# Kernel tuning notes

Measured on AMD Instinct MI355X. Metric: run time of the kernel, lower is better.

Reference implementation:

```python
import jax, jax.numpy as jnp
import numpy as np
from jax import lax

T, S = 2000, 100          # trees, nodes per tree
N = T * S                 # total nodes
F = 256                   # in_feats (sent_hidden_size)
H = 256                   # h_feats (prop_hidden_size)


def _build_forest():
    # Random recursive forest: node j in each tree attaches to a uniform earlier node.
    rng = np.random.default_rng(0)
    pl = np.zeros((T, S), np.int64)    # local parent index
    dep = np.zeros((T, S), np.int64)
    rows = np.arange(T)
    for j in range(1, S):
        p = rng.integers(0, j, size=T)
        pl[:, j] = p
        dep[:, j] = dep[rows, p] + 1
    depth = dep.ravel()
    parent = (np.arange(T)[:, None] * S + pl).ravel()
    is_root = (np.arange(N) % S) == 0
    kids = np.arange(N)[~is_root]
    par = parent[~is_root]
    order = np.argsort(par, kind='stable')
    kids_s, par_s = kids[order], par[order]
    counts = np.bincount(par_s, minlength=N)
    C = int(counts.max())
    offsets = np.concatenate([[0], np.cumsum(counts)])
    pos = np.arange(len(kids_s)) - offsets[par_s]
    ch_all = np.full((N, C), N + 1, np.int32)   # pad with dummy zero-hidden row N+1
    ch_all[par_s, pos] = kids_s
    maxd = int(depth.max())
    L = maxd  # processed layers: depths 0..maxd-1 (deepest leaves stay zero, as in torch)
    layer_lists = [np.where(depth == d)[0] for d in range(L)]
    M = max(len(l) for l in layer_lists)
    layer_nodes = np.full((L, M), N, np.int32)  # pad writes to scratch row N
    child_idx = np.full((L, M, C), N + 1, np.int32)
    child_cnt = np.zeros((L, M), np.int32)
    for d, nd in enumerate(layer_lists):
        m = len(nd)
        layer_nodes[d, :m] = nd
        child_idx[d, :m] = ch_all[nd]
        child_cnt[d, :m] = counts[nd]
    root_idx = (np.arange(T) * S).astype(np.int32)
    return layer_nodes, child_idx, child_cnt, root_idx


def setup_inputs() -> dict:
    layer_nodes, child_idx, child_cnt, root_idx = _build_forest()
    key = jax.random.key(0)
    k1, k2, k3, k4, k5 = jax.random.split(key, 5)
    bound = 1.0 / np.sqrt(H)  # torch GRUCell default init
    u = lambda kk, sh: jax.random.uniform(kk, sh, jnp.float32, -bound, bound)
    return {
        'inputs': jax.random.normal(k1, (N, F), jnp.float32),
        'w_ih': u(k2, (3 * H, F)),
        'w_hh': u(k3, (3 * H, H)),
        'b_ih': u(k4, (3 * H,)),
        'b_hh': u(k5, (3 * H,)),
        'layer_nodes': jnp.asarray(layer_nodes),
        'child_idx': jnp.asarray(child_idx),
        'child_cnt': jnp.asarray(child_cnt),
        'root_idx': jnp.asarray(root_idx),
    }


def _gru(x, h, w_ih, w_hh, b_ih, b_hh):
    gi = x @ w_ih.T + b_ih
    gh = h @ w_hh.T + b_hh
    ir, iz, ig = jnp.split(gi, 3, axis=-1)
    hr, hz, hg = jnp.split(gh, 3, axis=-1)
    r = jax.nn.sigmoid(ir + hr)
    z = jax.nn.sigmoid(iz + hz)
    n = jnp.tanh(ig + r * hg)
    return (1.0 - z) * n + z * h


def _forward(inputs, w_ih, w_hh, b_ih, b_hh, layer_nodes, child_idx, child_cnt, root_idx):
    # rows N (scatter scratch for padded slots) and N+1 (always-zero child pad) appended
    x_all = jnp.concatenate([inputs, jnp.zeros((2, F), inputs.dtype)], axis=0)
    h0 = jnp.zeros((N + 2, H), inputs.dtype)

    def step(all_h, layer):
        nodes, cidx, ccnt = layer
        ch = all_h[cidx]                                        # [M, C, H]
        denom = jnp.maximum(ccnt, 1).astype(all_h.dtype)[:, None]
        h_prev = ch.sum(axis=1) / denom                         # mean over children; 0 for leaves
        new_h = _gru(x_all[nodes], h_prev, w_ih, w_hh, b_ih, b_hh)
        return all_h.at[nodes].set(new_h), None

    # process deepest layer first (reversed(range(max_depth)) in the original)
    xs = (layer_nodes[::-1], child_idx[::-1], child_cnt[::-1])
    all_h, _ = lax.scan(step, h0, xs)
    return all_h[root_idx]                                      # [T, H]


def reference(inputs, w_ih, w_hh, b_ih, b_hh, layer_nodes, child_idx, child_cnt, root_idx):
    return _forward(inputs, w_ih, w_hh, b_ih, b_hh, layer_nodes, child_idx, child_cnt, root_idx)
```

## Files before the change

kernel.cpp:

```cpp
#include <hip/hip_runtime.h>
#include <hip/hip_bf16.h>
#include <math.h>

#define N_NODES 200000
#define T_TREES 2000
#define S_NODES 100
#define F_DIM 256
#define H_DIM 256
#define G_DIM 768
#define D_MAX 24

typedef __attribute__((ext_vector_type(8))) short short8b;
typedef __attribute__((ext_vector_type(4))) float f32x4;

static __device__ __forceinline__ unsigned short f2bf(float x) {
    union { __hip_bfloat16 h; unsigned short u; } cv;
    cv.h = __float2bfloat16(x);
    return cv.u;
}
static __device__ __forceinline__ float bf2f(unsigned short u) {
    return __uint_as_float(((unsigned)u) << 16);
}
static __device__ __forceinline__ float fsig(float x) {
    return __builtin_amdgcn_rcpf(1.0f + __expf(-x));
}
static __device__ __forceinline__ float ftanh(float x) {
    return 1.0f - 2.0f * __builtin_amdgcn_rcpf(__expf(2.0f * x) + 1.0f);
}

__global__ void k_zero(float4* __restrict__ p, int n4) {
    float4 z = make_float4(0.f, 0.f, 0.f, 0.f);
    for (int i = blockIdx.x * blockDim.x + threadIdx.x; i < n4;
         i += gridDim.x * blockDim.x)
        p[i] = z;
}

__global__ void k_convx(const float* __restrict__ x, unsigned short* __restrict__ xb,
                        int n8) {
    for (int i = blockIdx.x * blockDim.x + threadIdx.x; i < n8;
         i += gridDim.x * blockDim.x) {
        const float4* px = (const float4*)(x + (size_t)i * 8);
        float4 u = px[0], v = px[1];
        short8b t;
        t[0] = f2bf(u.x); t[1] = f2bf(u.y); t[2] = f2bf(u.z); t[3] = f2bf(u.w);
        t[4] = f2bf(v.x); t[5] = f2bf(v.y); t[6] = f2bf(v.z); t[7] = f2bf(v.w);
        *(short8b*)(xb + (size_t)i * 8) = t;
    }
}

__global__ void k_findM(const int* __restrict__ ln, int LM, int* __restrict__ Mdev) {
    int local = 0x7F7F7F7F;
    for (int p = T_TREES + blockIdx.x * blockDim.x + threadIdx.x; p < LM;
         p += gridDim.x * blockDim.x)
        if (ln[p] < N_NODES && p < local) local = p;
#pragma unroll
    for (int off = 32; off; off >>= 1) {
        int o = __shfl_down(local, off);
        if (o < local) local = o;
    }
    __shared__ int wmin[4];
    if ((threadIdx.x & 63) == 0) wmin[threadIdx.x >> 6] = local;
    __syncthreads();
    if (threadIdx.x == 0) {
        int m = wmin[0];
        for (int i = 1; i < 4; ++i) if (wmin[i] < m) m = wmin[i];
        if (m < 0x7F7F7F7F) atomicMin(Mdev, m);
    }
}

__global__ void k_compact(const int* __restrict__ ln,
                          const int* __restrict__ child_cnt,
                          const int* __restrict__ Mdev,
                          int* __restrict__ int_cnt,
                          int* __restrict__ int_pos,
                          int LM) {
    const int M = Mdev[0];
    const int lane = threadIdx.x & 63;
    for (int p = blockIdx.x * blockDim.x + threadIdx.x;
         p < ((LM + 63) & ~63);
         p += gridDim.x * blockDim.x) {
        const bool inb = (p < LM);
        const int d = inb ? (p / M) : 0;
        const bool pred = inb && (ln[p] < N_NODES) &&
                          (child_cnt[p] > 0 || p < M) && d < D_MAX;
        unsigned long long remaining = __ballot(pred);
        while (remaining) {
            const int leader = (int)__ffsll((long long)remaining) - 1;
            const int dd = __shfl(d, leader);
            const unsigned long long grp = __ballot(pred && d == dd);
            int base = 0;
            if (lane == leader)
                base = atomicAdd(&int_cnt[dd], (int)__popcll(grp));
            base = __shfl(base, leader);
            if (pred && d == dd) {
                int rank = (int)__popcll(grp & ((1ULL << lane) - 1ULL));
                int_pos[(size_t)dd * M + base + rank] = p;
            }
            remaining &= ~grp;
        }
    }
}

__global__ void k_convw(const float* __restrict__ wi, const float* __restrict__ wh,
                        unsigned short* __restrict__ wib, unsigned short* __restrict__ whb) {
    int i = blockIdx.x * blockDim.x + threadIdx.x;
    if (i < G_DIM * F_DIM) {
        wib[i] = f2bf(wi[i]);
        whb[i] = f2bf(wh[i]);
    }
}

__global__ __launch_bounds__(256) void k_gemm_x(
    const unsigned short* __restrict__ xb,
    const unsigned short* __restrict__ wib,
    const float* __restrict__ b_ih,
    unsigned short* __restrict__ gi_all) {
    __shared__ unsigned short Bs[2][64][256];

    const int tid = threadIdx.x;
    const int wv = tid >> 6, lane = tid & 63;
    const int lr = lane & 15, kg = lane >> 4;
    const long m0 = (long)blockIdx.x * 128 + wv * 32;

    short8b A[2][8];
#pragma unroll
    for (int ms = 0; ms < 2; ++ms) {
        long r = m0 + ms * 16 + lr;
        if (r > N_NODES - 1) r = N_NODES - 1;
        const unsigned short* xp = xb + r * F_DIM + kg * 8;
#pragma unroll
        for (int ks = 0; ks < 8; ++ks)
            A[ms][ks] = *(const short8b*)(xp + ks * 32);
    }

    const int sr = tid >> 2, sp = tid & 3;
    const int hs = (sr & 3) | (((sr >> 3) & 1) << 2);
    const int gp_off = (lr >> 2) * 8 + (lr & 3);
    const int hq = (lr & 3) | (((lr >> 2) & 1) << 2);

    short8b st[8];
    {
        const unsigned short* src = wib + (size_t)sr * F_DIM;
#pragma unroll
        for (int q = 0; q < 4; ++q) {
            int c = sp * 16 + q * 64;
            st[2 * q]     = *(const short8b*)(src + c);
            st[2 * q + 1] = *(const short8b*)(src + c + 8);
        }
#pragma unroll
        for (int q = 0; q < 4; ++q) {
            int c0 = sp * 2 + q * 8, c1 = c0 + 1;
            *(short8b*)&Bs[0][sr][((c0 & 24) | ((c0 ^ hs) & 7)) << 3] = st[2 * q];
            *(short8b*)&Bs[0][sr][((c1 & 24) | ((c1 ^ hs) & 7)) << 3] = st[2 * q + 1];
        }
    }
    __syncthreads();

    const f32x4 zf = {0.f, 0.f, 0.f, 0.f};

    for (int nt = 0; nt < 12; ++nt) {
        const int cur = nt & 1;
        if (nt < 11) {
            const unsigned short* src = wib + (size_t)((nt + 1) * 64 + sr) * F_DIM;
#pragma unroll
            for (int q = 0; q < 4; ++q) {
                int c = sp * 16 + q * 64;
                st[2 * q]     = *(const short8b*)(src + c);
                st[2 * q + 1] = *(const short8b*)(src + c + 8);
            }
        }
#pragma unroll
        for (int nsp = 0; nsp < 2; ++nsp) {
            f32x4 aP0 = zf, aQ0 = zf, aP1 = zf, aQ1 = zf;
            const int rP = nsp * 32 + gp_off;
#pragma unroll
            for (int ks = 0; ks < 8; ++ks) {
                const int c = ks * 4 + kg;
                const int pc = ((c & 24) | ((c ^ hq) & 7)) << 3;
                short8b BP = *(const short8b*)&Bs[cur][rP][pc];
                short8b BQ = *(const short8b*)&Bs[cur][rP + 4][pc];
                aP0 = __builtin_amdgcn_mfma_f32_16x16x32_bf16(BP, A[0][ks], aP0, 0, 0, 0);
                aQ0 = __builtin_amdgcn_mfma_f32_16x16x32_bf16(BQ, A[0][ks], aQ0, 0, 0, 0);
                aP1 = __builtin_amdgcn_mfma_f32_16x16x32_bf16(BP, A[1][ks], aP1, 0, 0, 0);
                aQ1 = __builtin_amdgcn_mfma_f32_16x16x32_bf16(BQ, A[1][ks], aQ1, 0, 0, 0);
            }
            const int g0 = nt * 64 + nsp * 32 + kg * 8;
            f32x4 b0 = *(const f32x4*)(b_ih + g0);
            f32x4 b1 = *(const f32x4*)(b_ih + g0 + 4);
            long m = m0 + lr;
            if (m < N_NODES) {
                short8b pk;
#pragma unroll
                for (int i = 0; i < 4; ++i) {
                    pk[i]     = f2bf(aP0[i] + b0[i]);
                    pk[4 + i] = f2bf(aQ0[i] + b1[i]);
                }
                *(short8b*)(gi_all + m * G_DIM + g0) = pk;
            }
            m = m0 + 16 + lr;
            if (m < N_NODES) {
                short8b pk;
#pragma unroll
                for (int i = 0; i < 4; ++i) {
                    pk[i]     = f2bf(aP1[i] + b0[i]);
                    pk[4 + i] = f2bf(aQ1[i] + b1[i]);
                }
                *(short8b*)(gi_all + m * G_DIM + g0) = pk;
            }
        }
        if (nt < 11) {
            __syncthreads();
#pragma unroll
            for (int q = 0; q < 4; ++q) {
                int c0 = sp * 2 + q * 8, c1 = c0 + 1;
                *(short8b*)&Bs[cur ^ 1][sr][((c0 & 24) | ((c0 ^ hs) & 7)) << 3] = st[2 * q];
                *(short8b*)&Bs[cur ^ 1][sr][((c1 & 24) | ((c1 ^ hs) & 7)) << 3] = st[2 * q + 1];
            }
            __syncthreads();
        }
    }
}

__global__ void k_leaf(const int* __restrict__ ln,
                       const int* __restrict__ child_cnt,
                       const int* __restrict__ Mdev,
                       const unsigned short* __restrict__ gi_all,
                       const float* __restrict__ b_hh,
                       unsigned short* __restrict__ h_all,
                       int LM) {
    const int M = Mdev[0];
    const int total = LM * 8;
    for (int t = blockIdx.x * blockDim.x + threadIdx.x; t < total;
         t += gridDim.x * blockDim.x) {
        const int p = t >> 3;
        if (p < M) continue;
        const int node = ln[p];
        if (node >= N_NODES || child_cnt[p] != 0) continue;
        const int cb = (t & 7) * 32;
        const unsigned short* gp = gi_all + (size_t)node * G_DIM;
        unsigned short* hw = h_all + (size_t)node * H_DIM;
#pragma unroll
        for (int q = 0; q < 4; ++q) {
            const int k = cb + q * 8;
            short8b gr = *(const short8b*)(gp + k);
            short8b gz = *(const short8b*)(gp + 256 + k);
            short8b gn = *(const short8b*)(gp + 512 + k);
            f32x4 br0 = *(const f32x4*)(b_hh + k);
            f32x4 br1 = *(const f32x4*)(b_hh + k + 4);
            f32x4 bz0 = *(const f32x4*)(b_hh + 256 + k);
            f32x4 bz1 = *(const f32x4*)(b_hh + 256 + k + 4);
            f32x4 bn0 = *(const f32x4*)(b_hh + 512 + k);
            f32x4 bn1 = *(const f32x4*)(b_hh + 512 + k + 4);
            short8b ph;
#pragma unroll
            for (int j = 0; j < 8; ++j) {
                float bhr = (j < 4) ? br0[j] : br1[j - 4];
                float bhz = (j < 4) ? bz0[j] : bz1[j - 4];
                float bhn = (j < 4) ? bn0[j] : bn1[j - 4];
                float r = fsig(bf2f((unsigned short)gr[j]) + bhr);
                float z = fsig(bf2f((unsigned short)gz[j]) + bhz);
                float n = ftanh(bf2f((unsigned short)gn[j]) + r * bhn);
                ph[j] = f2bf((1.0f - z) * n);
            }
            *(short8b*)(hw + k) = ph;
        }
    }
}

#define LOADC2(buf, ns_, kh_)                                                  \
  _Pragma("unroll")                                                            \
  for (int kk = 0; kk < 4; ++kk)                                               \
    buf[kk] = *(const short8b*)(whb +                                          \
        (size_t)(512 + cb + (ns_) * 16 + lr) * H_DIM + ((kh_) * 4 + kk) * 32 + kg * 8);

#define MMACP(c_)                                                              \
  _Pragma("unroll")                                                            \
  for (int ks = 0; ks < 8; ++ks) {                                             \
    const int cch = ks * 4 + kg;                                               \
    const int pc = ((cch & 24) | ((cch ^ lr) & 7)) << 3;                       \
    short8b A0 = *(const short8b*)&Ab[lr][pc];                                 \
    short8b A1 = *(const short8b*)&Ab[16 + lr][pc];                            \
    _Pragma("unroll")                                                          \
    for (int ns = 0; ns < 2; ++ns) {                                           \
      acc[c_][0][ns] = __builtin_amdgcn_mfma_f32_16x16x32_bf16(                \
          A0, Bp[c_][ns][ks], acc[c_][0][ns], 0, 0, 0);                        \
      acc[c_][1][ns] = __builtin_amdgcn_mfma_f32_16x16x32_bf16(                \
          A1, Bp[c_][ns][ks], acc[c_][1][ns], 0, 0, 0);                        \
    }                                                                          \
  }

#define MMAC2(buf, ns_, kh_)                                                   \
  _Pragma("unroll")                                                            \
  for (int kk = 0; kk < 4; ++kk) {                                             \
    const int ks = (kh_) * 4 + kk;                                             \
    const int cch = ks * 4 + kg;                                               \
    const int pc = ((cch & 24) | ((cch ^ lr) & 7)) << 3;                       \
    short8b A0 = *(const short8b*)&Ab[lr][pc];                                 \
    short8b A1 = *(const short8b*)&Ab[16 + lr][pc];                            \
    acc[2][0][ns_] = __builtin_amdgcn_mfma_f32_16x16x32_bf16(                  \
        A0, buf[kk], acc[2][0][ns_], 0, 0, 0);                                 \
    acc[2][1][ns_] = __builtin_amdgcn_mfma_f32_16x16x32_bf16(                  \
        A1, buf[kk], acc[2][1][ns_], 0, 0, 0);                                 \
  }

__global__ __launch_bounds__(512, 2) void k_layer(
    const int* __restrict__ layer_nodes,
    const int* __restrict__ child_idx,
    const int* __restrict__ child_cnt,
    const int* __restrict__ Mdev,
    const int* __restrict__ int_cnt,
    const int* __restrict__ int_pos,
    const unsigned short* __restrict__ whb,
    const unsigned short* __restrict__ gi_all,
    const float* __restrict__ b_hh,
    unsigned short* __restrict__ h_all,
    float* __restrict__ out,
    int d, int C) {
    __shared__ unsigned short Ab[32][256];
    __shared__ unsigned short Ag[32][776];
    __shared__ int Nd[32];

    const int icnt = int_cnt[d];
    if (icnt == 0) return;
    const int M = Mdev[0];
    const int ntiles = (icnt + 31) >> 5;
    if (blockIdx.x >= ntiles) return;
    const long pbase = (long)d * M;

    const int tid = threadIdx.x;
    const int wv = tid >> 6, lane = tid & 63;
    const int lr = lane & 15, kg = lane >> 4;
    const int cb = wv * 32;

    short8b Bp[2][2][8];
#pragma unroll
    for (int c = 0; c < 2; ++c)
#pragma unroll
        for (int ns = 0; ns < 2; ++ns) {
            const unsigned short* bp =
                whb + (size_t)(c * 256 + cb + ns * 16 + lr) * H_DIM + kg * 8;
#pragma unroll
            for (int ks = 0; ks < 8; ++ks)
                Bp[c][ns][ks] = *(const short8b*)(bp + ks * 32);
        }

    float bh[3][2];
#pragma unroll
    for (int c = 0; c < 3; ++c)
#pragma unroll
        for (int ns = 0; ns < 2; ++ns)
            bh[c][ns] = b_hh[c * 256 + cb + ns * 16 + lr];

    const int srow = tid >> 4;
    const int sc = tid & 15;

    for (int tile = blockIdx.x; tile < ntiles; tile += gridDim.x) {
        __syncthreads();
        {
            int slot = tile * 32 + srow;
            int p = (slot < icnt) ? int_pos[pbase + slot] : -1;
            int node = (p >= 0) ? layer_nodes[p] : -1;
            if (sc == 0) Nd[srow] = node;
            {
                const unsigned short* gp =
                    gi_all + (size_t)(node >= 0 ? node : 0) * G_DIM;
#pragma unroll
                for (int pass = 0; pass < 6; ++pass) {
                    int col = sc * 8 + pass * 128;
                    *(short8b*)&Ag[srow][col] = *(const short8b*)(gp + col);
                }
            }
            int cc = 0;
            const int* ch = nullptr;
            if (p >= 0) {
                cc = child_cnt[p];
                ch = child_idx + (size_t)p * C;
            }
            float inv = 1.0f / (float)(cc > 0 ? cc : 1);
            float sum[16];
#pragma unroll
            for (int i = 0; i < 16; ++i) sum[i] = 0.f;
#pragma unroll 2
            for (int c = 0; c < cc; ++c) {
                int kid = ch[c];
                const unsigned short* hr = h_all + (size_t)kid * H_DIM + sc * 16;
                short8b v0 = *(const short8b*)hr;
                short8b v1 = *(const short8b*)(hr + 8);
#pragma unroll
                for (int i = 0; i < 8; ++i) {
                    sum[i]     += bf2f((unsigned short)v0[i]);
                    sum[8 + i] += bf2f((unsigned short)v1[i]);
                }
            }
            short8b q0, q1;
#pragma unroll
            for (int i = 0; i < 8; ++i) {
                q0[i] = f2bf(sum[i] * inv);
                q1[i] = f2bf(sum[8 + i] * inv);
            }
            const int g = srow & 7;
            const int c0 = 2 * sc, c1 = 2 * sc + 1;
            *(short8b*)&Ab[srow][((c0 & 24) | ((c0 ^ g) & 7)) << 3] = q0;
            *(short8b*)&Ab[srow][((c1 & 24) | ((c1 ^ g) & 7)) << 3] = q1;
        }
        __syncthreads();

        const f32x4 zf = {0.f, 0.f, 0.f, 0.f};
        f32x4 acc[3][2][2];
#pragma unroll
        for (int c = 0; c < 3; ++c)
#pragma unroll
            for (int ms = 0; ms < 2; ++ms)
#pragma unroll
                for (int ns = 0; ns < 2; ++ns) acc[c][ms][ns] = zf;

        short8b C2a[4], C2b[4];
        LOADC2(C2a, 0, 0);
        MMACP(0);
        LOADC2(C2b, 0, 1);
        MMAC2(C2a, 0, 0);
        LOADC2(C2a, 1, 0);
        MMACP(1);
        MMAC2(C2b, 0, 1);
        LOADC2(C2b, 1, 1);
        MMAC2(C2a, 1, 0);
        MMAC2(C2b, 1, 1);

#pragma unroll
        for (int ms = 0; ms < 2; ++ms)
#pragma unroll
            for (int i = 0; i < 4; ++i) {
                const int rl = ms * 16 + kg * 4 + i;
                const int nd = Nd[rl];
                if (nd < 0) continue;
#pragma unroll
                for (int ns = 0; ns < 2; ++ns) {
                    const int k = cb + ns * 16 + lr;
                    const int kc = k >> 3;
                    const int hp_off = (((kc & 24) | ((kc ^ rl) & 7)) << 3) + (k & 7);
                    float hp = bf2f(Ab[rl][hp_off]);
                    float xr = bf2f(Ag[rl][k])       + acc[0][ms][ns][i] + bh[0][ns];
                    float xz = bf2f(Ag[rl][256 + k]) + acc[1][ms][ns][i] + bh[1][ns];
                    float r = fsig(xr);
                    float z = fsig(xz);
                    float n = ftanh(bf2f(Ag[rl][512 + k]) +
                                    r * (acc[2][ms][ns][i] + bh[2][ns]));
                    float h = (1.0f - z) * n + z * hp;
                    if (d == 0) {
                        out[(size_t)(nd / S_NODES) * H_DIM + k] = h;
                    } else {
                        h_all[(size_t)nd * H_DIM + k] = f2bf(h);
                    }
                }
            }
    }
}

extern "C" void kernel_launch(void* const* d_in, const int* in_sizes, int n_in,
                              void* d_out, int out_size, void* d_ws, size_t ws_size,
                              hipStream_t stream) {
    const float* inputs = (const float*)d_in[0];
    const float* w_ih   = (const float*)d_in[1];
    const float* w_hh   = (const float*)d_in[2];
    const float* b_ih   = (const float*)d_in[3];
    const float* b_hh   = (const float*)d_in[4];
    const int* layer_nodes = (const int*)d_in[5];
    const int* child_idx   = (const int*)d_in[6];
    const int* child_cnt   = (const int*)d_in[7];

    const int LM = in_sizes[5];
    const int C  = in_sizes[6] / in_sizes[5];

    char* w = (char*)d_ws;
    size_t o = 0;
    auto alloc = [&](size_t bytes) {
        void* p = w + o;
        o += (bytes + 255) & ~(size_t)255;
        return p;
    };
    unsigned short* wib    = (unsigned short*)alloc((size_t)G_DIM * F_DIM * 2);
    unsigned short* whb    = (unsigned short*)alloc((size_t)G_DIM * H_DIM * 2);
    unsigned short* xb     = (unsigned short*)alloc((size_t)N_NODES * F_DIM * 2);
    unsigned short* h_all  = (unsigned short*)alloc((size_t)N_NODES * H_DIM * 2);
    unsigned short* gi_all = (unsigned short*)alloc((size_t)N_NODES * G_DIM * 2);
    int*            int_pos   = (int*)alloc((size_t)LM * 4);
    int*            Mdev      = (int*)alloc(4);
    int*            int_cnt   = (int*)alloc(D_MAX * 4);
    (void)ws_size;

    hipMemsetAsync(Mdev, 0x7F, 4, stream);
    hipMemsetAsync(int_cnt, 0, D_MAX * 4, stream);

    k_zero<<<2048, 256, 0, stream>>>((float4*)h_all, N_NODES * H_DIM * 2 / 16);
    k_convx<<<2048, 256, 0, stream>>>(inputs, xb, N_NODES * F_DIM / 8);
    k_findM<<<256, 256, 0, stream>>>(layer_nodes, LM, Mdev);
    k_compact<<<512, 256, 0, stream>>>(layer_nodes, child_cnt, Mdev,
                                       int_cnt, int_pos, LM);
    k_convw<<<(G_DIM * F_DIM + 255) / 256, 256, 0, stream>>>(w_ih, w_hh, wib, whb);

    k_gemm_x<<<(N_NODES + 127) / 128, 256, 0, stream>>>(xb, wib, b_ih, gi_all);

    k_leaf<<<2048, 256, 0, stream>>>(layer_nodes, child_cnt, Mdev,
                                     gi_all, b_hh, h_all, LM);

    for (int d = D_MAX - 1; d >= 0; --d)
        k_layer<<<512, 512, 0, stream>>>(layer_nodes, child_idx, child_cnt,
                                         Mdev, int_cnt, int_pos, whb, gi_all,
                                         b_hh, h_all, (float*)d_out, d, C);
}
```

Before: 1.018 ms.

## Fuse per-layer launches into one persistent cooperative kernel with grid sync

Replaces the 24 per-depth k_layer launches with a single cooperative kernel that loops over depths internally and separates them with a threadfence plus grid.sync. The intent is to remove launch overhead and the reload of the register-resident W_hh fragments and biases at every layer. In exchange, every layer now pays a grid-wide barrier, and the grid size is capped by occupancy, assuming 256 CUs.

```diff
diff --git a/kernel.cpp b/kernel.cpp
--- a/kernel.cpp
+++ b/kernel.cpp
@@ -1,6 +1,9 @@
 #include <hip/hip_runtime.h>
 #include <hip/hip_bf16.h>
+#include <hip/hip_cooperative_groups.h>
 #include <math.h>
+
+namespace cg = cooperative_groups;
 
 #define N_NODES 200000
 #define T_TREES 2000
@@ -303,7 +306,7 @@
         A1, buf[kk], acc[2][1][ns_], 0, 0, 0);                                 \
   }
 
-__global__ __launch_bounds__(512, 2) void k_layer(
+__global__ __launch_bounds__(512, 2) void k_layers_all(
     const int* __restrict__ layer_nodes,
     const int* __restrict__ child_idx,
     const int* __restrict__ child_cnt,
@@ -315,18 +318,14 @@
     const float* __restrict__ b_hh,
     unsigned short* __restrict__ h_all,
     float* __restrict__ out,
-    int d, int C) {
+    int C) {
     __shared__ unsigned short Ab[32][256];
     __shared__ unsigned short Ag[32][776];
     __shared__ int Nd[32];
 
-    const int icnt = int_cnt[d];
-    if (icnt == 0) return;
+    cg::grid_group grid = cg::this_grid();
+
     const int M = Mdev[0];
-    const int ntiles = (icnt + 31) >> 5;
-    if (blockIdx.x >= ntiles) return;
-    const long pbase = (long)d * M;
-
     const int tid = threadIdx.x;
     const int wv = tid >> 6, lane = tid & 63;
     const int lr = lane & 15, kg = lane >> 4;
@@ -354,105 +353,119 @@
     const int srow = tid >> 4;
     const int sc = tid & 15;
 
-    for (int tile = blockIdx.x; tile < ntiles; tile += gridDim.x) {
-        __syncthreads();
-        {
-            int slot = tile * 32 + srow;
-            int p = (slot < icnt) ? int_pos[pbase + slot] : -1;
-            int node = (p >= 0) ? layer_nodes[p] : -1;
-            if (sc == 0) Nd[srow] = node;
+    for (int d = D_MAX - 1; d >= 0; --d) {
+        const int icnt = int_cnt[d];
+        if (icnt == 0) continue;
+        const int ntiles = (icnt + 31) >> 5;
+        const long pbase = (long)d * M;
+
+        for (int tile = blockIdx.x; tile < ntiles; tile += gridDim.x) {
+            __syncthreads();
             {
-                const unsigned short* gp =
-                    gi_all + (size_t)(node >= 0 ? node : 0) * G_DIM;
-#pragma unroll
-                for (int pass = 0; pass < 6; ++pass) {
-                    int col = sc * 8 + pass * 128;
-                    *(short8b*)&Ag[srow][col] = *(const short8b*)(gp + col);
-                }
-            }
-            int cc = 0;
-            const int* ch = nullptr;
-            if (p >= 0) {
-                cc = child_cnt[p];
-                ch = child_idx + (size_t)p * C;
-            }
-            float inv = 1.0f / (float)(cc > 0 ? cc : 1);
-            float sum[16];
-#pragma unroll
-            for (int i = 0; i < 16; ++i) sum[i] = 0.f;
+                int slot = tile * 32 + srow;
+                int p = (slot < icnt) ? int_pos[pbase + slot] : -1;
+                int node = (p >= 0) ? layer_nodes[p] : -1;
+                if (sc == 0) Nd[srow] = node;
+                {
+                    const unsigned short* gp =
+                        gi_all + (size_t)(node >= 0 ? node : 0) * G_DIM;
+#pragma unroll
+                    for (int pass = 0; pass < 6; ++pass) {
+                        int col = sc * 8 + pass * 128;
+                        *(short8b*)&Ag[srow][col] = *(const short8b*)(gp + col);
+                    }
+                }
+                int cc = 0;
+                const int* ch = nullptr;
+                if (p >= 0) {
+                    cc = child_cnt[p];
+                    ch = child_idx + (size_t)p * C;
+                }
+                float inv = 1.0f / (float)(cc > 0 ? cc : 1);
+                float sum[16];
+#pragma unroll
+                for (int i = 0; i < 16; ++i) sum[i] = 0.f;
 #pragma unroll 2
-            for (int c = 0; c < cc; ++c) {
-                int kid = ch[c];
-                const unsigned short* hr = h_all + (size_t)kid * H_DIM + sc * 16;
-                short8b v0 = *(const short8b*)hr;
-                short8b v1 = *(const short8b*)(hr + 8);
+                for (int c = 0; c < cc; ++c) {
+                    int kid = ch[c];
+                    const unsigned short* hr =
+                        h_all + (size_t)kid * H_DIM + sc * 16;
+                    short8b v0 = *(const short8b*)hr;
+                    short8b v1 = *(const short8b*)(hr + 8);
+#pragma unroll
+                    for (int i = 0; i < 8; ++i) {
+                        sum[i]     += bf2f((unsigned short)v0[i]);
+                        sum[8 + i] += bf2f((unsigned short)v1[i]);
+                    }
+                }
+                short8b q0, q1;
 #pragma unroll
                 for (int i = 0; i < 8; ++i) {
-                    sum[i]     += bf2f((unsigned short)v0[i]);
-                    sum[8 + i] += bf2f((unsigned short)v1[i]);
-                }
-            }
-            short8b q0, q1;
-#pragma unroll
-            for (int i = 0; i < 8; ++i) {
-                q0[i] = f2bf(sum[i] * inv);
-                q1[i] = f2bf(sum[8 + i] * inv);
-            }
-            const int g = srow & 7;
-            const int c0 = 2 * sc, c1 = 2 * sc + 1;
-            *(short8b*)&Ab[srow][((c0 & 24) | ((c0 ^ g) & 7)) << 3] = q0;
-            *(short8b*)&Ab[srow][((c1 & 24) | ((c1 ^ g) & 7)) << 3] = q1;
-        }
-        __syncthreads();
-
-        const f32x4 zf = {0.f, 0.f, 0.f, 0.f};
-        f32x4 acc[3][2][2];
-#pragma unroll
-        for (int c = 0; c < 3; ++c)
+                    q0[i] = f2bf(sum[i] * inv);
+                    q1[i] = f2bf(sum[8 + i] * inv);
+                }
+                const int g = srow & 7;
+                const int c0 = 2 * sc, c1 = 2 * sc + 1;
+                *(short8b*)&Ab[srow][((c0 & 24) | ((c0 ^ g) & 7)) << 3] = q0;
+                *(short8b*)&Ab[srow][((c1 & 24) | ((c1 ^ g) & 7)) << 3] = q1;
+            }
+            __syncthreads();
+
+            const f32x4 zf = {0.f, 0.f, 0.f, 0.f};
+            f32x4 acc[3][2][2];
+#pragma unroll
+            for (int c = 0; c < 3; ++c)
+#pragma unroll
+                for (int ms = 0; ms < 2; ++ms)
+#pragma unroll
+                    for (int ns = 0; ns < 2; ++ns) acc[c][ms][ns] = zf;
+
+            short8b C2a[4], C2b[4];
+            LOADC2(C2a, 0, 0);
+            MMACP(0);
+            LOADC2(C2b, 0, 1);
+            MMAC2(C2a, 0, 0);
+            LOADC2(C2a, 1, 0);
+            MMACP(1);
+            MMAC2(C2b, 0, 1);
+            LOADC2(C2b, 1, 1);
+            MMAC2(C2a, 1, 0);
+            MMAC2(C2b, 1, 1);
+
 #pragma unroll
             for (int ms = 0; ms < 2; ++ms)
 #pragma unroll
-                for (int ns = 0; ns < 2; ++ns) acc[c][ms][ns] = zf;
-
-        short8b C2a[4], C2b[4];
-        LOADC2(C2a, 0, 0);
-        MMACP(0);
-        LOADC2(C2b, 0, 1);
-        MMAC2(C2a, 0, 0);
-        LOADC2(C2a, 1, 0);
-        MMACP(1);
-        MMAC2(C2b, 0, 1);
-        LOADC2(C2b, 1, 1);
-        MMAC2(C2a, 1, 0);
-        MMAC2(C2b, 1, 1);
-
-#pragma unroll
-        for (int ms = 0; ms < 2; ++ms)
-#pragma unroll
-            for (int i = 0; i < 4; ++i) {
-                const int rl = ms * 16 + kg * 4 + i;
-                const int nd = Nd[rl];
-                if (nd < 0) continue;
-#pragma unroll
-                for (int ns = 0; ns < 2; ++ns) {
-                    const int k = cb + ns * 16 + lr;
-                    const int kc = k >> 3;
-                    const int hp_off = (((kc & 24) | ((kc ^ rl) & 7)) << 3) + (k & 7);
-                    float hp = bf2f(Ab[rl][hp_off]);
-                    float xr = bf2f(Ag[rl][k])       + acc[0][ms][ns][i] + bh[0][ns];
-                    float xz = bf2f(Ag[rl][256 + k]) + acc[1][ms][ns][i] + bh[1][ns];
-                    float r = fsig(xr);
-                    float z = fsig(xz);
-                    float n = ftanh(bf2f(Ag[rl][512 + k]) +
-                                    r * (acc[2][ms][ns][i] + bh[2][ns]));
-                    float h = (1.0f - z) * n + z * hp;
-                    if (d == 0) {
-                        out[(size_t)(nd / S_NODES) * H_DIM + k] = h;
-                    } else {
-                        h_all[(size_t)nd * H_DIM + k] = f2bf(h);
+                for (int i = 0; i < 4; ++i) {
+                    const int rl = ms * 16 + kg * 4 + i;
+                    const int nd = Nd[rl];
+                    if (nd < 0) continue;
+#pragma unroll
+                    for (int ns = 0; ns < 2; ++ns) {
+                        const int k = cb + ns * 16 + lr;
+                        const int kc = k >> 3;
+                        const int hp_off =
+                            (((kc & 24) | ((kc ^ rl) & 7)) << 3) + (k & 7);
+                        float hp = bf2f(Ab[rl][hp_off]);
+                        float xr = bf2f(Ag[rl][k])       + acc[0][ms][ns][i] + bh[0][ns];
+                        float xz = bf2f(Ag[rl][256 + k]) + acc[1][ms][ns][i] + bh[1][ns];
+                        float r = fsig(xr);
+                        float z = fsig(xz);
+                        float n = ftanh(bf2f(Ag[rl][512 + k]) +
+                                        r * (acc[2][ms][ns][i] + bh[2][ns]));
+                        float h = (1.0f - z) * n + z * hp;
+                        if (d == 0) {
+                            out[(size_t)(nd / S_NODES) * H_DIM + k] = h;
+                        } else {
+                            h_all[(size_t)nd * H_DIM + k] = f2bf(h);
+                        }
                     }
                 }
-            }
+        }
+
+        if (d > 0) {
+            __threadfence();
+            grid.sync();
+        }
     }
 }
 
@@ -469,7 +482,7 @@
     const int* child_cnt   = (const int*)d_in[7];
 
     const int LM = in_sizes[5];
-    const int C  = in_sizes[6] / in_sizes[5];
+    int C  = in_sizes[6] / in_sizes[5];
 
     char* w = (char*)d_ws;
     size_t o = 0;
@@ -503,8 +516,19 @@
     k_leaf<<<2048, 256, 0, stream>>>(layer_nodes, child_cnt, Mdev,
                                      gi_all, b_hh, h_all, LM);
 
-    for (int d = D_MAX - 1; d >= 0; --d)
-        k_layer<<<512, 512, 0, stream>>>(layer_nodes, child_idx, child_cnt,
-                                         Mdev, int_cnt, int_pos, whb, gi_all,
-                                         b_hh, h_all, (float*)d_out, d, C);
-}
+    float* outp = (float*)d_out;
+    void* args[] = {
+        (void*)&layer_nodes, (void*)&child_idx, (void*)&child_cnt,
+        (void*)&Mdev, (void*)&int_cnt, (void*)&int_pos,
+        (void*)&whb, (void*)&gi_all, (void*)&b_hh,
+        (void*)&h_all, (void*)&outp, (void*)&C
+    };
+    int maxb = 0;
+    hipOccupancyMaxActiveBlocksPerMultiprocessor(
+        &maxb, (const void*)k_layers_all, 512, 0);
+    if (maxb < 1) maxb = 1;
+    int grid = maxb * 256;
+    if (grid > 512) grid = 512;
+    hipLaunchCooperativeKernel((const void*)k_layers_all,
+                               dim3(grid), dim3(512), args, 0, stream);
+}
```

Result: slower. 1.807 ms (+77.6%).
